# Kernel optimization log

Hardware: AMD Instinct MI355X
Metric: run time of the kernel (lower is better)

Reference implementation:

```python
import jax, jax.numpy as jnp
import numpy as np

DIM = 256
NUM_HEADS = 8
CHUNK = 64
EPS = 1e-5


def layernorm(x, g, b):
    m = jnp.mean(x, axis=-1, keepdims=True)
    v = jnp.mean((x - m) ** 2, axis=-1, keepdims=True)
    return (x - m) / jnp.sqrt(v + EPS) * g + b


def setup_inputs() -> dict:
    key = jax.random.key(0)
    ks = jax.random.split(key, 12)
    B, C, H, W = 8, DIM, 64, 64
    s = 1.0 / np.sqrt(C)
    return {
        "x": jax.random.normal(ks[0], (B, C, H, W), jnp.float32),
        "CVA_input": jax.random.normal(ks[1], (B, C, H, W), jnp.float32),
        "qn_g": jnp.ones((C,), jnp.float32), "qn_b": jnp.zeros((C,), jnp.float32),
        "kn_g": jnp.ones((C,), jnp.float32), "kn_b": jnp.zeros((C,), jnp.float32),
        "vn_g": jnp.ones((C,), jnp.float32), "vn_b": jnp.zeros((C,), jnp.float32),
        "Wq": jax.random.normal(ks[2], (C, C), jnp.float32) * s,
        "bq": jnp.zeros((C,), jnp.float32),
        "Wk": jax.random.normal(ks[3], (C, C), jnp.float32) * s,
        "bk": jnp.zeros((C,), jnp.float32),
        "Wv": jax.random.normal(ks[4], (C, C), jnp.float32) * s,
        "bv": jnp.zeros((C,), jnp.float32),
        "Wp": jax.random.normal(ks[5], (C, C), jnp.float32) * s,
        "bp": jnp.zeros((C,), jnp.float32),
    }


def reference(x, CVA_input, qn_g, qn_b, kn_g, kn_b, vn_g, vn_b,
              Wq, bq, Wk, bk, Wv, bv, Wp, bp):
    B, C, H, W = x.shape
    N = H * W
    nh = NUM_HEADS
    hd = C // nh
    scale = hd ** -0.5
    nc = N // CHUNK  # number of non-overlapping chunks

    xs = x.reshape(B, C, N).transpose(0, 2, 1)          # [B,N,C]
    cva = CVA_input.reshape(B, -1, C)                    # [B,N,C] (raw reshape, as in torch)

    def heads(t):  # [B,N,C] -> [B,nh,nc,CHUNK,hd]
        return t.reshape(B, N, nh, hd).transpose(0, 2, 1, 3).reshape(B, nh, nc, CHUNK, hd)

    q = heads(layernorm(cva, qn_g, qn_b) @ Wq + bq)
    k = heads(layernorm(cva, kn_g, kn_b) @ Wk + bk)
    v = heads(layernorm(xs, vn_g, vn_b) @ Wv + bv)

    # block-local attention: each chunk attends only within itself
    scores = jnp.einsum('bhncd,bhnkd->bhnck', q, k) * scale  # [B,nh,nc,CHUNK,CHUNK]
    probs = jax.nn.softmax(scores, axis=-1)
    o = jnp.einsum('bhnck,bhnkd->bhncd', probs, v)           # [B,nh,nc,CHUNK,hd]

    o = o.reshape(B, nh, N, hd).transpose(0, 2, 1, 3).reshape(B, N, C)
    out = o @ Wp + bp                                        # [B,N,C]
    return out.transpose(0, 2, 1).reshape(B, C, H, W)
```

## Files before the change

### kernel.cpp

```cpp
#include <hip/hip_runtime.h>
#include <hip/hip_bf16.h>

#define NTOK 4096
#define BATCH 8
#define NROWS (BATCH * NTOK)

typedef __attribute__((ext_vector_type(8))) _Float16 hfx8;
typedef __attribute__((ext_vector_type(4))) short bfx4;
typedef __attribute__((ext_vector_type(4))) float f32x4;

__device__ __forceinline__ short f2h(float f) {
    _Float16 h = (_Float16)f;
    return __builtin_bit_cast(short, h);
}
__device__ __forceinline__ unsigned pk2h(float a, float b) {
    return (unsigned)(unsigned short)f2h(a) | ((unsigned)(unsigned short)f2h(b) << 16);
}

__device__ __forceinline__ int aswz(int row, int col) {
    return (row * 256 + col) ^ ((row & 7) << 3);
}
__device__ __forceinline__ int xoidx(int row, int col) {
    return row * 32 + ((((col >> 3) + (row >> 1)) & 3) << 3) + (col & 7);
}

#define MFMA16(a, b, c) __builtin_amdgcn_mfma_f32_16x16x32_f16(a, b, c, 0, 0, 0)
#define LGKM0()                                              \
    do {                                                     \
        asm volatile("s_waitcnt lgkmcnt(0)" ::: "memory");   \
        __builtin_amdgcn_sched_barrier(0);                   \
    } while (0)

__global__ __launch_bounds__(256) void prep_w(
    const float* __restrict__ Wq, const float* __restrict__ Wk,
    const float* __restrict__ Wv, const float* __restrict__ Wp,
    const float* __restrict__ qg, const float* __restrict__ qb,
    const float* __restrict__ kg, const float* __restrict__ kb,
    const float* __restrict__ vg, const float* __restrict__ vb,
    short* __restrict__ wt, float* __restrict__ bbp) {
    int m = blockIdx.x;
    int ci0 = blockIdx.y * 16;
    const float *W, *g, *be;
    float scale = 1.0f;
    if (m == 0)      { W = Wq; g = qg; be = qb; scale = 0.17677669529663687f; }
    else if (m == 1) { W = Wk; g = kg; be = kb; }
    else if (m == 2) { W = Wv; g = vg; be = vb; }
    else             { W = Wp; g = nullptr; be = nullptr; }
    __shared__ float tile[16][257];
    int t = threadIdx.x;
#pragma unroll
    for (int i = 0; i < 16; i++)
        tile[i][t] = W[(size_t)(ci0 + i) * 256 + t];
    __syncthreads();
    float p = 0.f;
    if (be) {
#pragma unroll
        for (int i = 0; i < 16; i++) p += be[ci0 + i] * tile[i][t];
    }
    bbp[(m * 16 + blockIdx.y) * 256 + t] = p;
    short* WT = wt + m * 65536 + t * 256 + ci0;
    short o0[8], o1[8];
#pragma unroll
    for (int j = 0; j < 8; j++) {
        float gv = g ? g[ci0 + j] : 1.0f;
        o0[j] = f2h(scale * gv * tile[j][t]);
    }
#pragma unroll
    for (int j = 0; j < 8; j++) {
        float gv = g ? g[ci0 + 8 + j] : 1.0f;
        o1[j] = f2h(scale * gv * tile[8 + j][t]);
    }
#pragma unroll
    for (int j = 0; j < 8; j++) { WT[j] = o0[j]; WT[8 + j] = o1[j]; }
}

__global__ __launch_bounds__(256) void prep_b(
    const float* __restrict__ bq, const float* __restrict__ bk,
    const float* __restrict__ bv, const float* __restrict__ bp,
    const float* __restrict__ bbp, float* __restrict__ bb) {
    int m = blockIdx.x, t = threadIdx.x;
    const float* bias = (m == 0) ? bq : (m == 1) ? bk : (m == 2) ? bv : bp;
    float scale = (m == 0) ? 0.17677669529663687f : 1.0f;
    float s = bias[t];
#pragma unroll
    for (int i = 0; i < 16; i++) s += bbp[(m * 16 + i) * 256 + t];
    bb[m * 256 + t] = scale * s;
}

__global__ __launch_bounds__(512, 4) void mega(const float* __restrict__ x,
                                               const float* __restrict__ cva,
                                               const short* __restrict__ wt,
                                               const float* __restrict__ bb,
                                               float* __restrict__ out) {
    int id = blockIdx.x;
    int b = id >> 6, ch = id & 63;
    int t = threadIdx.x, w = t >> 6, l = t & 63, c = l & 15, g = l >> 4;

    __shared__ short A[64 * 256];
    __shared__ short xo[8][2048];
    __shared__ float red[8][64][2];
    short* S = A + w * 2048;

    const float* xb   = x + (size_t)b * 1048576 + ch * 64;
    const float* cvab = cva + (size_t)(b * 4096 + ch * 64) * 256;

    {
        int r16 = g;
        float fv[2][16];
#pragma unroll
        for (int p2 = 0; p2 < 2; p2++) {
            int row = w * 8 + p2 * 4 + r16;
#pragma unroll
            for (int i = 0; i < 4; i++) {
                float4 v4 = *reinterpret_cast<const float4*>(
                    cvab + (size_t)row * 256 + c * 16 + i * 4);
                fv[p2][i * 4 + 0] = v4.x;
                fv[p2][i * 4 + 1] = v4.y;
                fv[p2][i * 4 + 2] = v4.z;
                fv[p2][i * 4 + 3] = v4.w;
            }
        }
        float xg[32];
#pragma unroll
        for (int i = 0; i < 32; i++) xg[i] = xb[(size_t)(w * 32 + i) * 4096 + l];

#pragma unroll
        for (int p2 = 0; p2 < 2; p2++) {
            int row = w * 8 + p2 * 4 + r16;
            float s = 0.f, q2 = 0.f;
#pragma unroll
            for (int i = 0; i < 16; i++) {
                s += fv[p2][i];
                q2 += fv[p2][i] * fv[p2][i];
            }
            s += __shfl_xor(s, 1);  q2 += __shfl_xor(q2, 1);
            s += __shfl_xor(s, 2);  q2 += __shfl_xor(q2, 2);
            s += __shfl_xor(s, 4);  q2 += __shfl_xor(q2, 4);
            s += __shfl_xor(s, 8);  q2 += __shfl_xor(q2, 8);
            float mean = s * (1.0f / 256.0f);
            float rstd = rsqrtf(q2 * (1.0f / 256.0f) - mean * mean + 1e-5f);
            short o0[8], o1[8];
#pragma unroll
            for (int jj = 0; jj < 8; jj++) {
                o0[jj] = f2h((fv[p2][jj] - mean) * rstd);
                o1[jj] = f2h((fv[p2][8 + jj] - mean) * rstd);
            }
            short* d0 = A + aswz(row, c * 16);
            short* d1 = A + aswz(row, c * 16 + 8);
#pragma unroll
            for (int jj = 0; jj < 8; jj++) { d0[jj] = o0[jj]; d1[jj] = o1[jj]; }
        }

        float s = 0.f, q2 = 0.f;
#pragma unroll
        for (int i = 0; i < 32; i++) { s += xg[i]; q2 += xg[i] * xg[i]; }
        red[w][l][0] = s;
        red[w][l][1] = q2;
        __syncthreads();

        float s2 = 0.f, q22 = 0.f;
#pragma unroll
        for (int j2 = 0; j2 < 8; j2++) { s2 += red[j2][l][0]; q22 += red[j2][l][1]; }
        float xmean = s2 * (1.0f / 256.0f);
        float xrstd = rsqrtf(q22 * (1.0f / 256.0f) - xmean * xmean + 1e-5f);
#pragma unroll
        for (int i2 = 0; i2 < 4; i2++) {
            short* dd = xo[w] + xoidx(l, i2 * 8);
#pragma unroll
            for (int jj = 0; jj < 8; jj++) dd[jj] = f2h((xg[i2 * 8 + jj] - xmean) * xrstd);
        }
    }

    f32x4 qa[4][2] = {}, ka[4][2] = {};
    {
        const short* wq0 = wt + (size_t)(w * 32 + c) * 256 + g * 8;
        const short* wq1 = wq0 + 16 * 256;
        const short* wk0 = wq0 + 65536;
        const short* wk1 = wq1 + 65536;
#pragma unroll
        for (int ks = 0; ks < 8; ks++) {
            hfx8 af[4];
#pragma unroll
            for (int m = 0; m < 4; m++)
                af[m] = *reinterpret_cast<const hfx8*>(A + aswz(m * 16 + c, ks * 32 + g * 8));
            hfx8 q0 = *reinterpret_cast<const hfx8*>(wq0 + ks * 32);
            hfx8 q1 = *reinterpret_cast<const hfx8*>(wq1 + ks * 32);
            hfx8 k0 = *reinterpret_cast<const hfx8*>(wk0 + ks * 32);
            hfx8 k1 = *reinterpret_cast<const hfx8*>(wk1 + ks * 32);
#pragma unroll
            for (int m = 0; m < 4; m++) {
                qa[m][0] = MFMA16(af[m], q0, qa[m][0]);
                qa[m][1] = MFMA16(af[m], q1, qa[m][1]);
                ka[m][0] = MFMA16(af[m], k0, ka[m][0]);
                ka[m][1] = MFMA16(af[m], k1, ka[m][1]);
            }
        }
    }
    __syncthreads();


    hfx8 qf[4];
    {
        float b0 = bb[w * 32 + c], b1 = bb[w * 32 + 16 + c];
#pragma unroll
        for (int th = 0; th < 2; th++) {
#pragma unroll
            for (int m2 = 0; m2 < 2; m2++)
#pragma unroll
                for (int j = 0; j < 4; j++) {
                    S[(m2 * 16 + g * 4 + j) * 40 + c]      = f2h(qa[th * 2 + m2][0][j] + b0);
                    S[(m2 * 16 + g * 4 + j) * 40 + 16 + c] = f2h(qa[th * 2 + m2][1][j] + b1);
                }
            LGKM0();
#pragma unroll
            for (int np = 0; np < 2; np++)
                qf[th * 2 + np] = *reinterpret_cast<const hfx8*>(S + (np * 16 + c) * 40 + g * 8);
            LGKM0();
        }
    }

    hfx8 kf[4];
    {
        float b0 = bb[256 + w * 32 + c], b1 = bb[256 + w * 32 + 16 + c];
#pragma unroll
        for (int th = 0; th < 2; th++) {
#pragma unroll
            for (int m2 = 0; m2 < 2; m2++)
#pragma unroll
                for (int j = 0; j < 4; j++) {
                    S[(m2 * 16 + g * 4 + j) * 40 + c]      = f2h(ka[th * 2 + m2][0][j] + b0);
                    S[(m2 * 16 + g * 4 + j) * 40 + 16 + c] = f2h(ka[th * 2 + m2][1][j] + b1);
                }
            LGKM0();
#pragma unroll
            for (int np = 0; np < 2; np++)
                kf[th * 2 + np] = *reinterpret_cast<const hfx8*>(S + (np * 16 + c) * 40 + g * 8);
            LGKM0();
        }
    }

    f32x4 sa[4][4] = {};
#pragma unroll
    for (int m = 0; m < 4; m++)
#pragma unroll
        for (int np = 0; np < 4; np++)
            sa[m][np] = MFMA16(kf[m], qf[np], sa[m][np]);

    float rs[4];
#pragma unroll
    for (int np = 0; np < 4; np++) {
        float mx = sa[0][np][0];
#pragma unroll
        for (int m = 0; m < 4; m++)
#pragma unroll
            for (int j = 0; j < 4; j++) mx = fmaxf(mx, sa[m][np][j]);
        mx = fmaxf(mx, __shfl_xor(mx, 16));
        mx = fmaxf(mx, __shfl_xor(mx, 32));
        float sum = 0.f;
#pragma unroll
        for (int m = 0; m < 4; m++)
#pragma unroll
            for (int j = 0; j < 4; j++) {
                float e = __expf(sa[m][np][j] - mx);
                sa[m][np][j] = e;
                sum += e;
            }
        sum += __shfl_xor(sum, 16);
        sum += __shfl_xor(sum, 32);
        rs[np] = 1.0f / sum;
    }

    unsigned Pp[4][4][2];
#pragma unroll
    for (int m = 0; m < 4; m++)
#pragma unroll
        for (int np = 0; np < 4; np++) {
            Pp[m][np][0] = pk2h(sa[m][np][0], sa[m][np][1]);
            Pp[m][np][1] = pk2h(sa[m][np][2], sa[m][np][3]);
        }

    f32x4 va[4][2] = {};
    {
        const short* w0 = wt + 2 * 65536 + (size_t)(w * 32 + c) * 256 + g * 8;
        const short* w1 = w0 + 16 * 256;
#pragma unroll
        for (int ks = 0; ks < 8; ks++) {
            hfx8 af[4];
#pragma unroll
            for (int m = 0; m < 4; m++)
                af[m] = *reinterpret_cast<const hfx8*>(xo[ks] + xoidx(m * 16 + c, g * 8));
            hfx8 v0 = *reinterpret_cast<const hfx8*>(w0 + ks * 32);
            hfx8 v1 = *reinterpret_cast<const hfx8*>(w1 + ks * 32);
#pragma unroll
            for (int m = 0; m < 4; m++) {
                va[m][0] = MFMA16(af[m], v0, va[m][0]);
                va[m][1] = MFMA16(af[m], v1, va[m][1]);
            }
        }
    }

    hfx8 vf[2][2];
    {
        float b0 = bb[512 + w * 32 + c], b1 = bb[512 + w * 32 + 16 + c];
#pragma unroll
        for (int ks = 0; ks < 2; ks++) {
#pragma unroll
            for (int m2 = 0; m2 < 2; m2++) {
                int m = ks * 2 + m2;
                bfx4 t0, t1;
#pragma unroll
                for (int j = 0; j < 4; j++) {
                    t0[j] = f2h(va[m][0][j] + b0);
                    t1[j] = f2h(va[m][1][j] + b1);
                }
                *reinterpret_cast<bfx4*>(S + c * 40 + m2 * 16 + g * 4)        = t0;
                *reinterpret_cast<bfx4*>(S + (16 + c) * 40 + m2 * 16 + g * 4) = t1;
            }
            LGKM0();
#pragma unroll
            for (int mD = 0; mD < 2; mD++)
                vf[ks][mD] = *reinterpret_cast<const hfx8*>(S + (mD * 16 + c) * 40 + g * 8);
            LGKM0();
        }
    }

    f32x4 oa[2][4] = {};
#pragma unroll
    for (int ks = 0; ks < 2; ks++) {
#pragma unroll
        for (int th = 0; th < 2; th++) {
#pragma unroll
            for (int m2 = 0; m2 < 2; m2++)
#pragma unroll
                for (int np = 0; np < 2; np++) {
                    *reinterpret_cast<unsigned*>(S + (np * 16 + c) * 40 + m2 * 16 + g * 4)     = Pp[ks * 2 + m2][th * 2 + np][0];
                    *reinterpret_cast<unsigned*>(S + (np * 16 + c) * 40 + m2 * 16 + g * 4 + 2) = Pp[ks * 2 + m2][th * 2 + np][1];
                }
            LGKM0();
            hfx8 pf[2];
#pragma unroll
            for (int np = 0; np < 2; np++)
                pf[np] = *reinterpret_cast<const hfx8*>(S + (np * 16 + c) * 40 + g * 8);
            LGKM0();
#pragma unroll
            for (int mD = 0; mD < 2; mD++)
#pragma unroll
                for (int np = 0; np < 2; np++)
                    oa[mD][th * 2 + np] = MFMA16(vf[ks][mD], pf[np], oa[mD][th * 2 + np]);
        }
    }
    __syncthreads();

#pragma unroll
    for (int mD = 0; mD < 2; mD++)
#pragma unroll
        for (int np = 0; np < 4; np++) {
            bfx4 o4;
#pragma unroll
            for (int j = 0; j < 4; j++) o4[j] = f2h(oa[mD][np][j] * rs[np]);
            *reinterpret_cast<bfx4*>(xo[w] + xoidx(np * 16 + c, mD * 16 + g * 4)) = o4;
        }
    __syncthreads();

    {
        f32x4 pa[4][2] = {};
        const short* w0 = wt + 3 * 65536 + (size_t)(w * 32 + c) * 256 + g * 8;
        const short* w1 = w0 + 16 * 256;
#pragma unroll
        for (int ks = 0; ks < 8; ks++) {
            hfx8 af[4];
#pragma unroll
            for (int m = 0; m < 4; m++)
                af[m] = *reinterpret_cast<const hfx8*>(xo[ks] + xoidx(m * 16 + c, g * 8));
            hfx8 p0 = *reinterpret_cast<const hfx8*>(w0 + ks * 32);
            hfx8 p1 = *reinterpret_cast<const hfx8*>(w1 + ks * 32);
#pragma unroll
            for (int m = 0; m < 4; m++) {
                pa[m][0] = MFMA16(af[m], p0, pa[m][0]);
                pa[m][1] = MFMA16(af[m], p1, pa[m][1]);
            }
        }
        float* outb = out + (size_t)b * 1048576 + ch * 64;
#pragma unroll
        for (int p = 0; p < 2; p++) {
            int co = w * 32 + p * 16 + c;
            float bvv = bb[768 + co];
            float* op = outb + (size_t)co * 4096 + g * 4;
#pragma unroll
            for (int m = 0; m < 4; m++) {
                float4 st;
                st.x = pa[m][p][0] + bvv;
                st.y = pa[m][p][1] + bvv;
                st.z = pa[m][p][2] + bvv;
                st.w = pa[m][p][3] + bvv;
                *reinterpret_cast<float4*>(op + m * 16) = st;
            }
        }
    }
}

extern "C" void kernel_launch(void* const* d_in, const int* in_sizes, int n_in,
                              void* d_out, int out_size, void* d_ws, size_t ws_size,
                              hipStream_t stream) {
    const float* x   = (const float*)d_in[0];
    const float* cva = (const float*)d_in[1];
    const float* qg  = (const float*)d_in[2];
    const float* qb  = (const float*)d_in[3];
    const float* kg  = (const float*)d_in[4];
    const float* kb  = (const float*)d_in[5];
    const float* vg  = (const float*)d_in[6];
    const float* vb  = (const float*)d_in[7];
    const float* Wq  = (const float*)d_in[8];
    const float* bq  = (const float*)d_in[9];
    const float* Wk  = (const float*)d_in[10];
    const float* bk  = (const float*)d_in[11];
    const float* Wv  = (const float*)d_in[12];
    const float* bv  = (const float*)d_in[13];
    const float* Wp  = (const float*)d_in[14];
    const float* bp  = (const float*)d_in[15];
    float* out = (float*)d_out;
    char* ws = (char*)d_ws;

    short* wt  = (short*)(ws);
    float* bb  = (float*)(ws + 4 * 65536 * sizeof(short));
    float* bbp = bb + 1024;

    prep_w<<<dim3(4, 16), 256, 0, stream>>>(Wq, Wk, Wv, Wp, qg, qb, kg, kb, vg, vb,
                                            wt, bbp);
    prep_b<<<4, 256, 0, stream>>>(bq, bk, bv, bp, bbp, bb);

    mega<<<512, 512, 0, stream>>>(x, cva, wt, bb, out);
}
```

Before: 67.83 us.

## Keep attention operands in registers via transposed MFMA layouts, drop LDS round-trips

The Q/K projections now swap the MFMA operand order, producing transposed accumulators that feed 16x16x16 f16 MFMAs directly for QK^T and PV. This removes the per-wave LDS staging (write, wait, reread) previously used to reshape Q, K, V and P fragments. Softmax normalization is folded into P before the PV product rather than applied to the output. The attention output is written into the A buffer for the output projection, and one __syncthreads is dropped. This trades the LDS shuffles for more, smaller K=16 MFMA instructions, and rounding P to fp16 after normalization slightly changes numerics.

```diff
diff --git a/kernel.cpp b/kernel.cpp
--- a/kernel.cpp
+++ b/kernel.cpp
@@ -6,16 +6,13 @@
 #define NROWS (BATCH * NTOK)
 
 typedef __attribute__((ext_vector_type(8))) _Float16 hfx8;
-typedef __attribute__((ext_vector_type(4))) short bfx4;
+typedef __attribute__((ext_vector_type(4))) _Float16 hfx4;
 typedef __attribute__((ext_vector_type(4))) float f32x4;
 
 __device__ __forceinline__ short f2h(float f) {
     _Float16 h = (_Float16)f;
     return __builtin_bit_cast(short, h);
 }
-__device__ __forceinline__ unsigned pk2h(float a, float b) {
-    return (unsigned)(unsigned short)f2h(a) | ((unsigned)(unsigned short)f2h(b) << 16);
-}
 
 __device__ __forceinline__ int aswz(int row, int col) {
     return (row * 256 + col) ^ ((row & 7) << 3);
@@ -24,12 +21,8 @@
     return row * 32 + ((((col >> 3) + (row >> 1)) & 3) << 3) + (col & 7);
 }
 
-#define MFMA16(a, b, c) __builtin_amdgcn_mfma_f32_16x16x32_f16(a, b, c, 0, 0, 0)
-#define LGKM0()                                              \
-    do {                                                     \
-        asm volatile("s_waitcnt lgkmcnt(0)" ::: "memory");   \
-        __builtin_amdgcn_sched_barrier(0);                   \
-    } while (0)
+#define MFMA32(a, b, c) __builtin_amdgcn_mfma_f32_16x16x32_f16(a, b, c, 0, 0, 0)
+#define MFMA16(a, b, c) __builtin_amdgcn_mfma_f32_16x16x16f16(a, b, c, 0, 0, 0)
 
 __global__ __launch_bounds__(256) void prep_w(
     const float* __restrict__ Wq, const float* __restrict__ Wk,
@@ -99,7 +92,6 @@
     __shared__ short A[64 * 256];
     __shared__ short xo[8][2048];
     __shared__ float red[8][64][2];
-    short* S = A + w * 2048;
 
     const float* xb   = x + (size_t)b * 1048576 + ch * 64;
     const float* cvab = cva + (size_t)(b * 4096 + ch * 64) * 256;
@@ -171,7 +163,7 @@
         }
     }
 
-    f32x4 qa[4][2] = {}, ka[4][2] = {};
+    f32x4 qa[2][4] = {}, ka[2][4] = {};
     {
         const short* wq0 = wt + (size_t)(w * 32 + c) * 256 + g * 8;
         const short* wq1 = wq0 + 16 * 256;
@@ -181,203 +173,145 @@
         for (int ks = 0; ks < 8; ks++) {
             hfx8 af[4];
 #pragma unroll
-            for (int m = 0; m < 4; m++)
-                af[m] = *reinterpret_cast<const hfx8*>(A + aswz(m * 16 + c, ks * 32 + g * 8));
+            for (int nt = 0; nt < 4; nt++)
+                af[nt] = *reinterpret_cast<const hfx8*>(A + aswz(nt * 16 + c, ks * 32 + g * 8));
             hfx8 q0 = *reinterpret_cast<const hfx8*>(wq0 + ks * 32);
             hfx8 q1 = *reinterpret_cast<const hfx8*>(wq1 + ks * 32);
             hfx8 k0 = *reinterpret_cast<const hfx8*>(wk0 + ks * 32);
             hfx8 k1 = *reinterpret_cast<const hfx8*>(wk1 + ks * 32);
 #pragma unroll
-            for (int m = 0; m < 4; m++) {
-                qa[m][0] = MFMA16(af[m], q0, qa[m][0]);
-                qa[m][1] = MFMA16(af[m], q1, qa[m][1]);
-                ka[m][0] = MFMA16(af[m], k0, ka[m][0]);
-                ka[m][1] = MFMA16(af[m], k1, ka[m][1]);
+            for (int nt = 0; nt < 4; nt++) {
+                qa[0][nt] = MFMA32(q0, af[nt], qa[0][nt]);
+                qa[1][nt] = MFMA32(q1, af[nt], qa[1][nt]);
+                ka[0][nt] = MFMA32(k0, af[nt], ka[0][nt]);
+                ka[1][nt] = MFMA32(k1, af[nt], ka[1][nt]);
             }
         }
     }
     __syncthreads();
 
-
-    hfx8 qf[4];
-    {
-        float b0 = bb[w * 32 + c], b1 = bb[w * 32 + 16 + c];
-#pragma unroll
-        for (int th = 0; th < 2; th++) {
-#pragma unroll
-            for (int m2 = 0; m2 < 2; m2++)
-#pragma unroll
-                for (int j = 0; j < 4; j++) {
-                    S[(m2 * 16 + g * 4 + j) * 40 + c]      = f2h(qa[th * 2 + m2][0][j] + b0);
-                    S[(m2 * 16 + g * 4 + j) * 40 + 16 + c] = f2h(qa[th * 2 + m2][1][j] + b1);
-                }
-            LGKM0();
-#pragma unroll
-            for (int np = 0; np < 2; np++)
-                qf[th * 2 + np] = *reinterpret_cast<const hfx8*>(S + (np * 16 + c) * 40 + g * 8);
-            LGKM0();
-        }
-    }
-
-    hfx8 kf[4];
-    {
-        float b0 = bb[256 + w * 32 + c], b1 = bb[256 + w * 32 + 16 + c];
-#pragma unroll
-        for (int th = 0; th < 2; th++) {
-#pragma unroll
-            for (int m2 = 0; m2 < 2; m2++)
-#pragma unroll
-                for (int j = 0; j < 4; j++) {
-                    S[(m2 * 16 + g * 4 + j) * 40 + c]      = f2h(ka[th * 2 + m2][0][j] + b0);
-                    S[(m2 * 16 + g * 4 + j) * 40 + 16 + c] = f2h(ka[th * 2 + m2][1][j] + b1);
-                }
-            LGKM0();
-#pragma unroll
-            for (int np = 0; np < 2; np++)
-                kf[th * 2 + np] = *reinterpret_cast<const hfx8*>(S + (np * 16 + c) * 40 + g * 8);
-            LGKM0();
-        }
-    }
-
-    f32x4 sa[4][4] = {};
-#pragma unroll
-    for (int m = 0; m < 4; m++)
-#pragma unroll
-        for (int np = 0; np < 4; np++)
-            sa[m][np] = MFMA16(kf[m], qf[np], sa[m][np]);
+    hfx4 qTf[2][4], kTf[2][4];
+#pragma unroll
+    for (int mt = 0; mt < 2; mt++) {
+        f32x4 bq4 = *reinterpret_cast<const f32x4*>(bb + w * 32 + mt * 16 + g * 4);
+        f32x4 bk4 = *reinterpret_cast<const f32x4*>(bb + 256 + w * 32 + mt * 16 + g * 4);
+#pragma unroll
+        for (int nt = 0; nt < 4; nt++)
+#pragma unroll
+            for (int j = 0; j < 4; j++) {
+                qTf[mt][nt][j] = (_Float16)(qa[mt][nt][j] + bq4[j]);
+                kTf[mt][nt][j] = (_Float16)(ka[mt][nt][j] + bk4[j]);
+            }
+    }
+
+    f32x4 saT[4][4] = {};
+#pragma unroll
+    for (int mt = 0; mt < 2; mt++)
+#pragma unroll
+        for (int ntk = 0; ntk < 4; ntk++)
+#pragma unroll
+            for (int ntq = 0; ntq < 4; ntq++)
+                saT[ntk][ntq] = MFMA16(kTf[mt][ntk], qTf[mt][ntq], saT[ntk][ntq]);
 
     float rs[4];
 #pragma unroll
-    for (int np = 0; np < 4; np++) {
-        float mx = sa[0][np][0];
-#pragma unroll
-        for (int m = 0; m < 4; m++)
-#pragma unroll
-            for (int j = 0; j < 4; j++) mx = fmaxf(mx, sa[m][np][j]);
+    for (int ntq = 0; ntq < 4; ntq++) {
+        float mx = saT[0][ntq][0];
+#pragma unroll
+        for (int ntk = 0; ntk < 4; ntk++)
+#pragma unroll
+            for (int j = 0; j < 4; j++) mx = fmaxf(mx, saT[ntk][ntq][j]);
         mx = fmaxf(mx, __shfl_xor(mx, 16));
         mx = fmaxf(mx, __shfl_xor(mx, 32));
         float sum = 0.f;
 #pragma unroll
-        for (int m = 0; m < 4; m++)
+        for (int ntk = 0; ntk < 4; ntk++)
 #pragma unroll
             for (int j = 0; j < 4; j++) {
-                float e = __expf(sa[m][np][j] - mx);
-                sa[m][np][j] = e;
+                float e = __expf(saT[ntk][ntq][j] - mx);
+                saT[ntk][ntq][j] = e;
                 sum += e;
             }
         sum += __shfl_xor(sum, 16);
         sum += __shfl_xor(sum, 32);
-        rs[np] = 1.0f / sum;
-    }
-
-    unsigned Pp[4][4][2];
-#pragma unroll
-    for (int m = 0; m < 4; m++)
-#pragma unroll
-        for (int np = 0; np < 4; np++) {
-            Pp[m][np][0] = pk2h(sa[m][np][0], sa[m][np][1]);
-            Pp[m][np][1] = pk2h(sa[m][np][2], sa[m][np][3]);
-        }
+        rs[ntq] = 1.0f / sum;
+    }
+
+    hfx4 Pf[4][4];
+#pragma unroll
+    for (int ks = 0; ks < 4; ks++)
+#pragma unroll
+        for (int mo = 0; mo < 4; mo++)
+#pragma unroll
+            for (int j = 0; j < 4; j++)
+                Pf[ks][mo][j] = (_Float16)(saT[ks][mo][j] * rs[mo]);
 
     f32x4 va[4][2] = {};
     {
-        const short* w0 = wt + 2 * 65536 + (size_t)(w * 32 + c) * 256 + g * 8;
-        const short* w1 = w0 + 16 * 256;
+        const short* wv0 = wt + 2 * 65536 + (size_t)(w * 32 + c) * 256 + g * 8;
+        const short* wv1 = wv0 + 16 * 256;
 #pragma unroll
         for (int ks = 0; ks < 8; ks++) {
             hfx8 af[4];
 #pragma unroll
             for (int m = 0; m < 4; m++)
                 af[m] = *reinterpret_cast<const hfx8*>(xo[ks] + xoidx(m * 16 + c, g * 8));
-            hfx8 v0 = *reinterpret_cast<const hfx8*>(w0 + ks * 32);
-            hfx8 v1 = *reinterpret_cast<const hfx8*>(w1 + ks * 32);
+            hfx8 v0 = *reinterpret_cast<const hfx8*>(wv0 + ks * 32);
+            hfx8 v1 = *reinterpret_cast<const hfx8*>(wv1 + ks * 32);
 #pragma unroll
             for (int m = 0; m < 4; m++) {
-                va[m][0] = MFMA16(af[m], v0, va[m][0]);
-                va[m][1] = MFMA16(af[m], v1, va[m][1]);
-            }
-        }
-    }
-
-    hfx8 vf[2][2];
-    {
-        float b0 = bb[512 + w * 32 + c], b1 = bb[512 + w * 32 + 16 + c];
-#pragma unroll
-        for (int ks = 0; ks < 2; ks++) {
-#pragma unroll
-            for (int m2 = 0; m2 < 2; m2++) {
-                int m = ks * 2 + m2;
-                bfx4 t0, t1;
-#pragma unroll
-                for (int j = 0; j < 4; j++) {
-                    t0[j] = f2h(va[m][0][j] + b0);
-                    t1[j] = f2h(va[m][1][j] + b1);
-                }
-                *reinterpret_cast<bfx4*>(S + c * 40 + m2 * 16 + g * 4)        = t0;
-                *reinterpret_cast<bfx4*>(S + (16 + c) * 40 + m2 * 16 + g * 4) = t1;
-            }
-            LGKM0();
-#pragma unroll
-            for (int mD = 0; mD < 2; mD++)
-                vf[ks][mD] = *reinterpret_cast<const hfx8*>(S + (mD * 16 + c) * 40 + g * 8);
-            LGKM0();
-        }
-    }
-
-    f32x4 oa[2][4] = {};
-#pragma unroll
-    for (int ks = 0; ks < 2; ks++) {
-#pragma unroll
-        for (int th = 0; th < 2; th++) {
-#pragma unroll
-            for (int m2 = 0; m2 < 2; m2++)
-#pragma unroll
-                for (int np = 0; np < 2; np++) {
-                    *reinterpret_cast<unsigned*>(S + (np * 16 + c) * 40 + m2 * 16 + g * 4)     = Pp[ks * 2 + m2][th * 2 + np][0];
-                    *reinterpret_cast<unsigned*>(S + (np * 16 + c) * 40 + m2 * 16 + g * 4 + 2) = Pp[ks * 2 + m2][th * 2 + np][1];
-                }
-            LGKM0();
-            hfx8 pf[2];
-#pragma unroll
-            for (int np = 0; np < 2; np++)
-                pf[np] = *reinterpret_cast<const hfx8*>(S + (np * 16 + c) * 40 + g * 8);
-            LGKM0();
-#pragma unroll
-            for (int mD = 0; mD < 2; mD++)
-#pragma unroll
-                for (int np = 0; np < 2; np++)
-                    oa[mD][th * 2 + np] = MFMA16(vf[ks][mD], pf[np], oa[mD][th * 2 + np]);
-        }
-    }
+                va[m][0] = MFMA32(af[m], v0, va[m][0]);
+                va[m][1] = MFMA32(af[m], v1, va[m][1]);
+            }
+        }
+    }
+
+    hfx4 vf[4][2];
+    {
+        float bv0 = bb[512 + w * 32 + c], bv1 = bb[512 + w * 32 + 16 + c];
+#pragma unroll
+        for (int m = 0; m < 4; m++)
+#pragma unroll
+            for (int j = 0; j < 4; j++) {
+                vf[m][0][j] = (_Float16)(va[m][0][j] + bv0);
+                vf[m][1][j] = (_Float16)(va[m][1][j] + bv1);
+            }
+    }
+
+    f32x4 oacc[4][2] = {};
+#pragma unroll
+    for (int ks = 0; ks < 4; ks++)
+#pragma unroll
+        for (int mo = 0; mo < 4; mo++)
+#pragma unroll
+            for (int no = 0; no < 2; no++)
+                oacc[mo][no] = MFMA16(Pf[ks][mo], vf[ks][no], oacc[mo][no]);
+
+#pragma unroll
+    for (int mo = 0; mo < 4; mo++)
+#pragma unroll
+        for (int no = 0; no < 2; no++)
+#pragma unroll
+            for (int j = 0; j < 4; j++)
+                A[aswz(mo * 16 + 4 * g + j, w * 32 + no * 16 + c)] = f2h(oacc[mo][no][j]);
     __syncthreads();
 
-#pragma unroll
-    for (int mD = 0; mD < 2; mD++)
-#pragma unroll
-        for (int np = 0; np < 4; np++) {
-            bfx4 o4;
-#pragma unroll
-            for (int j = 0; j < 4; j++) o4[j] = f2h(oa[mD][np][j] * rs[np]);
-            *reinterpret_cast<bfx4*>(xo[w] + xoidx(np * 16 + c, mD * 16 + g * 4)) = o4;
-        }
-    __syncthreads();
-
     {
         f32x4 pa[4][2] = {};
-        const short* w0 = wt + 3 * 65536 + (size_t)(w * 32 + c) * 256 + g * 8;
-        const short* w1 = w0 + 16 * 256;
+        const short* wp0 = wt + 3 * 65536 + (size_t)(w * 32 + c) * 256 + g * 8;
+        const short* wp1 = wp0 + 16 * 256;
 #pragma unroll
         for (int ks = 0; ks < 8; ks++) {
             hfx8 af[4];
 #pragma unroll
             for (int m = 0; m < 4; m++)
-                af[m] = *reinterpret_cast<const hfx8*>(xo[ks] + xoidx(m * 16 + c, g * 8));
-            hfx8 p0 = *reinterpret_cast<const hfx8*>(w0 + ks * 32);
-            hfx8 p1 = *reinterpret_cast<const hfx8*>(w1 + ks * 32);
+                af[m] = *reinterpret_cast<const hfx8*>(A + aswz(m * 16 + c, ks * 32 + g * 8));
+            hfx8 p0 = *reinterpret_cast<const hfx8*>(wp0 + ks * 32);
+            hfx8 p1 = *reinterpret_cast<const hfx8*>(wp1 + ks * 32);
 #pragma unroll
             for (int m = 0; m < 4; m++) {
-                pa[m][0] = MFMA16(af[m], p0, pa[m][0]);
-                pa[m][1] = MFMA16(af[m], p1, pa[m][1]);
+                pa[m][0] = MFMA32(af[m], p0, pa[m][0]);
+                pa[m][1] = MFMA32(af[m], p1, pa[m][1]);
             }
         }
         float* outb = out + (size_t)b * 1048576 + ch * 64;
```

Result: no change. 67.58 us (-0.4%).
